# Kernel optimization log

Measured on AMD Instinct MI355X. Metric: run time of the kernel, lower is better.

The kernel has to match this reference:

```python
import jax, jax.numpy as jnp
import numpy as np

N = 500000      # gaussians
D = 256         # d_model
H = 8           # heads
DFF = 1024      # ffn hidden
L = 2           # encoder layers
VS = 0.0625     # voxel_size
MR = 10         # multires (both embedders)
EPS = 1e-5      # layernorm eps


def _embed(x, nf):
    freqs = 2.0 ** jnp.arange(nf, dtype=x.dtype)
    xf = x[..., None, :] * freqs[:, None]                  # [..., F, 3]
    sc = jnp.stack([jnp.sin(xf), jnp.cos(xf)], axis=-2)    # [..., F, 2, 3]
    return jnp.concatenate([x, sc.reshape(*x.shape[:-1], nf * 2 * 3)], axis=-1)


def _ln(x, w, b):
    m = x.mean(-1, keepdims=True)
    v = ((x - m) ** 2).mean(-1, keepdims=True)
    return (x - m) / jnp.sqrt(v + EPS) * w + b


def _mha(x, wi, bi, wo, bo):
    U, d = x.shape
    dh = d // H
    qkv = x @ wi.T + bi                                    # [U, 3d]
    q, k, v = jnp.split(qkv, 3, axis=-1)
    sp = lambda t: t.reshape(U, H, dh).transpose(1, 0, 2)  # [H, U, dh]
    q, k, v = sp(q), sp(k), sp(v)
    scale = 1.0 / jnp.sqrt(jnp.asarray(dh, x.dtype))
    attn = jax.nn.softmax(jnp.einsum('hqd,hkd->hqk', q, k) * scale, axis=-1)
    o = jnp.einsum('hqk,hkd->hqd', attn, v).transpose(1, 0, 2).reshape(U, d)
    return o @ wo.T + bo


def setup_inputs() -> dict:
    key = jax.random.key(0)
    ks = jax.random.split(key, 24)
    centres = jax.random.uniform(ks[0], (N, 3), dtype=jnp.float32)
    feats = jax.random.normal(ks[1], (N, D), dtype=jnp.float32)
    # voxelize + unique (data-dependent -> precompute, round() has zero grad anyway)
    vp = np.round(np.asarray(centres) / VS) * VS
    _, inv = np.unique(vp, axis=0, return_inverse=True)
    inv = inv.reshape(-1)
    U = int(inv.max()) + 1
    s = 0.02
    rn = lambda k, shp: jax.random.normal(k, shp, dtype=jnp.float32) * s
    PE = MR * 2 * 3 + 3  # 63
    return dict(
        gaussian_centres=centres,
        gaussian_features=feats,
        inverse_indices=jnp.asarray(inv, jnp.int32),
        num_unique=U,
        in_proj_w=rn(ks[2], (L, 3 * D, D)), in_proj_b=rn(ks[3], (L, 3 * D)),
        out_proj_w=rn(ks[4], (L, D, D)), out_proj_b=rn(ks[5], (L, D)),
        lin1_w=rn(ks[6], (L, DFF, D)), lin1_b=rn(ks[7], (L, DFF)),
        lin2_w=rn(ks[8], (L, D, DFF)), lin2_b=rn(ks[9], (L, D)),
        norm1_w=jnp.ones((L, D), jnp.float32), norm1_b=jnp.zeros((L, D), jnp.float32),
        norm2_w=jnp.ones((L, D), jnp.float32), norm2_b=jnp.zeros((L, D), jnp.float32),
        pe_w1=rn(ks[10], (D, PE)), pe_b1=rn(ks[11], (D,)),
        pe_w2=rn(ks[12], (D, D)), pe_b2=rn(ks[13], (D,)),
        dm_w1=rn(ks[14], (D, D + PE)), dm_b1=rn(ks[15], (D,)),
        dm_w2=rn(ks[16], (D, D)), dm_b2=rn(ks[17], (D,)),
    )


def reference(gaussian_centres, gaussian_features, inverse_indices, num_unique,
              in_proj_w, in_proj_b, out_proj_w, out_proj_b,
              lin1_w, lin1_b, lin2_w, lin2_b,
              norm1_w, norm1_b, norm2_w, norm2_b,
              pe_w1, pe_b1, pe_w2, pe_b2,
              dm_w1, dm_b1, dm_w2, dm_b2):
    # 1-4: voxelize + segment-sum features per unique voxel
    vp = jnp.round(gaussian_centres / VS) * VS
    agg = jax.ops.segment_sum(gaussian_features, inverse_indices, num_segments=num_unique)  # [U, D]
    uv = jnp.zeros((num_unique, 3), gaussian_centres.dtype).at[inverse_indices].set(vp)     # unique voxel coords
    # learnable positional encoding MLP
    pe = _embed(uv, MR)
    pe = jax.nn.leaky_relu(pe @ pe_w1.T + pe_b1, 0.01) @ pe_w2.T + pe_b2
    # transformer encoder (post-LN, relu, eval mode -> no dropout)
    x = agg + pe
    for l in range(L):
        x = _ln(x + _mha(x, in_proj_w[l], in_proj_b[l], out_proj_w[l], out_proj_b[l]),
                norm1_w[l], norm1_b[l])
        ff = jax.nn.relu(x @ lin1_w[l].T + lin1_b[l]) @ lin2_w[l].T + lin2_b[l]
        x = _ln(x + ff, norm2_w[l], norm2_b[l])
    # 6-7: gather back to per-gaussian rows
    rec = x[inverse_indices]                                # [N, D]
    # delta MLP: cat([pos_encoding, features])
    d_in = jnp.concatenate([_embed(gaussian_centres, MR), rec], axis=-1)
    delta = jax.nn.leaky_relu(d_in @ dm_w1.T + dm_b1, 0.01) @ dm_w2.T + dm_b2
    return rec + delta
```

## Files before the change

### kernel.cpp

```cpp
#include <hip/hip_runtime.h>
#include <math.h>

#define NG   500000
#define DM   256
#define NH   8
#define DHD  32
#define DFF  1024
#define NLAY 2
#define PED  63
#define VSF  0.0625f
#define EPSF 1e-5f
#define UP   4928
#define MAXU 4913
#define NQT  77
#define NDBLK 7813
#define SCL  0.17677669529663687f

typedef short bf16x8 __attribute__((ext_vector_type(8)));
typedef float f32x4 __attribute__((ext_vector_type(4)));

__device__ __forceinline__ float lrelu(float v){ return v >= 0.f ? v : 0.01f*v; }

__device__ __forceinline__ short f2b(float f){
  unsigned u = __float_as_uint(f);
  return (short)((u + 0x7fffu + ((u >> 16) & 1u)) >> 16);
}

__device__ __forceinline__ f32x4 mfma16(bf16x8 a, bf16x8 b, f32x4 c){
  return __builtin_amdgcn_mfma_f32_16x16x32_bf16(a, b, c, 0, 0, 0);
}

__device__ __forceinline__ float embed_elem(float cx, float cy, float cz, int j){
  if (j == 0) return cx;
  if (j == 1) return cy;
  if (j == 2) return cz;
  int q = j - 3;
  int f = q / 6;
  int r = q - f*6;
  int c = r % 3;
  float base = (c==0)?cx:((c==1)?cy:cz);
  float xf = base * (float)(1u << f);
  return (r < 3) ? sinf(xf) : cosf(xf);
}

__device__ __forceinline__ float wred(float v){
  #pragma unroll
  for (int o = 32; o > 0; o >>= 1) v += __shfl_xor(v, o);
  return v;
}

__global__ void zero_kernel(int* p, int n){
  int i = blockIdx.x*blockDim.x + threadIdx.x;
  if (i < n) p[i] = 0;
}

__global__ void prep_kernel(const float* __restrict__ centres, const int* __restrict__ inv,
                            int* __restrict__ counts, float* __restrict__ uv){
  for (int i = blockIdx.x*blockDim.x + threadIdx.x; i < NG; i += gridDim.x*blockDim.x){
    int v = inv[i];
    atomicAdd(&counts[v], 1);
    float vx = rintf(centres[i*3]   * 16.f) * VSF;
    float vy = rintf(centres[i*3+1] * 16.f) * VSF;
    float vz = rintf(centres[i*3+2] * 16.f) * VSF;
    uv[v*3] = vx; uv[v*3+1] = vy; uv[v*3+2] = vz;
  }
}

__global__ void scan_kernel(const int* __restrict__ counts, int* __restrict__ offs,
                            const int* __restrict__ pU){
  const int U = *pU;
  const int CH = 8;
  __shared__ int tot[1024];
  int tid = threadIdx.x;
  int base = tid * CH;
  int c[CH];
  int s = 0;
  #pragma unroll
  for (int i = 0; i < CH; ++i){
    int idx = base + i;
    int v = (idx < U) ? counts[idx] : 0;
    c[i] = s;
    s += v;
  }
  tot[tid] = s;
  __syncthreads();
  for (int o = 1; o < 1024; o <<= 1){
    int v = 0;
    if (tid >= o) v = tot[tid - o];
    __syncthreads();
    tot[tid] += v;
    __syncthreads();
  }
  int excl = tot[tid] - s;
  #pragma unroll
  for (int i = 0; i < CH; ++i){
    int idx = base + i;
    if (idx < U) offs[idx] = excl + c[i];
  }
}

__global__ void scatter_kernel(const int* __restrict__ inv, const int* __restrict__ offs,
                               int* __restrict__ cursor, int* __restrict__ gidx){
  for (int i = blockIdx.x*blockDim.x + threadIdx.x; i < NG; i += gridDim.x*blockDim.x){
    int v = inv[i];
    int p = atomicAdd(&cursor[v], 1);
    gidx[offs[v] + p] = i;
  }
}

__global__ void cvt_weights(const float* __restrict__ ipw, const float* __restrict__ opw,
                            const float* __restrict__ l1w, const float* __restrict__ l2w,
                            const float* __restrict__ dw1, const float* __restrict__ dw2,
                            short* ipwb, short* opwb, short* l1wb, short* l2wb,
                            short* dw2b, short* dw1bb, short* dw1ab){
  int i = blockIdx.x*256 + threadIdx.x;
  switch (blockIdx.y){
    case 0: if (i < 2*768*256)  ipwb[i] = f2b(ipw[i]); break;
    case 1: if (i < 2*256*256)  opwb[i] = f2b(opw[i]); break;
    case 2: if (i < 2*1024*256) l1wb[i] = f2b(l1w[i]); break;
    case 3: if (i < 2*256*1024) l2wb[i] = f2b(l2w[i]); break;
    case 4: if (i < 256*256)    dw2b[i] = f2b(dw2[i]); break;
    case 5: if (i < 256*256){ int r = i>>8, c = i&255; dw1bb[i] = f2b(dw1[r*319 + 63 + c]); } break;
    case 6: if (i < 256*64){  int r = i>>6, c = i&63;  dw1ab[i] = f2b(c < 63 ? dw1[r*319 + c] : 0.f); } break;
  }
}

__global__ __launch_bounds__(256) void agg_pe_kernel(const float* __restrict__ feats,
   const int* __restrict__ gidx, const int* __restrict__ offs, const int* __restrict__ counts,
   const float* __restrict__ uv, const float* __restrict__ pw1, const float* __restrict__ pb1,
   const float* __restrict__ pw2, const float* __restrict__ pb2,
   float* __restrict__ x, const int* __restrict__ pU){
  const int U = *pU;
  __shared__ int gl[512];
  __shared__ __align__(16) float4 red[256];
  __shared__ __align__(16) float e[PED];
  __shared__ __align__(16) float h[DM];
  const int t = threadIdx.x;
  const int c4 = t & 63;
  const int rr = t >> 6;
  for (int u = blockIdx.x; u < U; u += gridDim.x){
    const int o0 = offs[u], cnt = counts[u];
    float4 s = {0.f,0.f,0.f,0.f};
    for (int base = 0; base < cnt; base += 512){
      const int cc = min(cnt - base, 512);
      __syncthreads();
      for (int j = t; j < cc; j += 256) gl[j] = gidx[o0 + base + j];
      __syncthreads();
      int j = rr;
      for (; j + 8 <= cc; j += 8){
        const int r0 = gl[j], r1 = gl[j+4];
        float4 v0 = *reinterpret_cast<const float4*>(&feats[(size_t)r0*DM + c4*4]);
        float4 v1 = *reinterpret_cast<const float4*>(&feats[(size_t)r1*DM + c4*4]);
        s.x += v0.x + v1.x; s.y += v0.y + v1.y;
        s.z += v0.z + v1.z; s.w += v0.w + v1.w;
      }
      for (; j < cc; j += 4){
        float4 v0 = *reinterpret_cast<const float4*>(&feats[(size_t)gl[j]*DM + c4*4]);
        s.x += v0.x; s.y += v0.y; s.z += v0.z; s.w += v0.w;
      }
    }
    red[t] = s;
    if (t < PED)
      e[t] = embed_elem(uv[u*3], uv[u*3+1], uv[u*3+2], t);
    __syncthreads();
    if (rr == 0){
      float4 a = red[c4], b = red[64+c4], c = red[128+c4], d = red[192+c4];
      a.x += b.x + c.x + d.x; a.y += b.y + c.y + d.y;
      a.z += b.z + c.z + d.z; a.w += b.w + c.w + d.w;
      red[c4] = a;
    }
    __syncthreads();
    const float sum = reinterpret_cast<const float*>(red)[t];
    float a1 = pb1[t];
    const float* w1 = pw1 + t*PED;
    for (int k = 0; k < PED; ++k) a1 += w1[k]*e[k];
    h[t] = lrelu(a1);
    __syncthreads();
    float a2 = pb2[t];
    const float* w2 = pw2 + (size_t)t*DM;
    for (int k = 0; k < DM; k += 4){
      float4 w = *reinterpret_cast<const float4*>(w2+k);
      float4 hv = *reinterpret_cast<const float4*>(&h[k]);
      a2 += w.x*hv.x + w.y*hv.y + w.z*hv.z + w.w*hv.w;
    }
    x[(size_t)u*DM + t] = sum + a2;
    __syncthreads();
  }
}

template<int ACT, bool HASRES>
__global__ __launch_bounds__(256) void gemm_bf(const float* __restrict__ A,
    const short* __restrict__ Bbf, const float* __restrict__ bias,
    const float* __restrict__ res, float* __restrict__ C,
    const int K, const int Nn, const int* __restrict__ pU){
  const int M = *pU;
  const int r0 = blockIdx.x * 64;
  if (r0 >= M) return;
  const int n0 = blockIdx.y * 64;
  __shared__ __align__(16) short Al[64*32];
  const int tid = threadIdx.x;
  const int wid = tid >> 6, lane = tid & 63;
  const int l15 = lane & 15, l4 = lane >> 4;
  f32x4 acc[4];
  #pragma unroll
  for (int nt = 0; nt < 4; ++nt) acc[nt] = (f32x4){0.f,0.f,0.f,0.f};
  const int nk = K >> 5;
  const int srow = tid >> 2, se8 = (tid & 3) * 8;
  const int arowc = min(r0 + srow, M-1);
  for (int kc = 0; kc < nk; ++kc){
    {
      const float* ap = A + (size_t)arowc*K + kc*32 + se8;
      f32x4 a0 = *(const f32x4*)ap;
      f32x4 a1 = *(const f32x4*)(ap + 4);
      bf16x8 av;
      av[0]=f2b(a0[0]); av[1]=f2b(a0[1]); av[2]=f2b(a0[2]); av[3]=f2b(a0[3]);
      av[4]=f2b(a1[0]); av[5]=f2b(a1[1]); av[6]=f2b(a1[2]); av[7]=f2b(a1[3]);
      *(bf16x8*)&Al[(srow*32 + se8) ^ ((srow & 7) << 3)] = av;
    }
    __syncthreads();
    const int ar = 16*wid + l15;
    bf16x8 af = *(const bf16x8*)&Al[(ar*32 + 8*l4) ^ ((ar & 7) << 3)];
    #pragma unroll
    for (int nt = 0; nt < 4; ++nt){
      const short* bp = Bbf + (size_t)(n0 + 16*nt + l15)*K + kc*32 + 8*l4;
      bf16x8 bfr = *(const bf16x8*)bp;
      acc[nt] = mfma16(af, bfr, acc[nt]);
    }
    __syncthreads();
  }
  #pragma unroll
  for (int nt = 0; nt < 4; ++nt){
    const int col = n0 + 16*nt + l15;
    const float bv = bias[col];
    #pragma unroll
    for (int r = 0; r < 4; ++r){
      const int row = r0 + 16*wid + 4*l4 + r;
      if (row < M){
        float v = acc[nt][r] + bv;
        if (ACT == 1) v = fmaxf(v, 0.f);
        if (HASRES) v += res[(size_t)row*Nn + col];
        C[(size_t)row*Nn + col] = v;
      }
    }
  }
}

__global__ __launch_bounds__(256) void attn_mfma(const float* __restrict__ qkv,
                                                 float* __restrict__ y, const int* __restrict__ pU){
  const int U = *pU;
  const int bid = blockIdx.x;
  const int h = bid & 7, qt = bid >> 3;
  const int q0 = qt * 64;
  const int tid = threadIdx.x;
  const int wid = tid >> 6, lane = tid & 63;
  const int l15 = lane & 15, l4 = lane >> 4;
  __shared__ __align__(16) short Kl[64*32];
  __shared__ __align__(16) short Vt[32*64];
  __shared__ __align__(16) short Pl[4][64*16];

  const int qrow = min(q0 + 16*wid + l15, U-1);
  const float* qp = qkv + (size_t)qrow*768 + h*DHD + 8*l4;
  bf16x8 qf;
  {
    f32x4 q0v = *(const f32x4*)qp;
    f32x4 q1v = *(const f32x4*)(qp + 4);
    qf[0]=f2b(q0v[0]*SCL); qf[1]=f2b(q0v[1]*SCL); qf[2]=f2b(q0v[2]*SCL); qf[3]=f2b(q0v[3]*SCL);
    qf[4]=f2b(q1v[0]*SCL); qf[5]=f2b(q1v[1]*SCL); qf[6]=f2b(q1v[2]*SCL); qf[7]=f2b(q1v[3]*SCL);
  }
  f32x4 o0 = (f32x4){0.f,0.f,0.f,0.f}, o1 = (f32x4){0.f,0.f,0.f,0.f};
  float mrun = -INFINITY, lrun = 0.f;
  const int srow = tid >> 2, se8 = (tid & 3) * 8;
  const int ntile = (U + 63) >> 6;
  for (int kt = 0; kt < ntile; ++kt){
    const int kb = kt * 64;
    {
      const int krow = min(kb + srow, U-1);
      const float* kp = qkv + (size_t)krow*768 + DM + h*DHD + se8;
      f32x4 k0 = *(const f32x4*)kp;
      f32x4 k1 = *(const f32x4*)(kp + 4);
      bf16x8 kv;
      kv[0]=f2b(k0[0]); kv[1]=f2b(k0[1]); kv[2]=f2b(k0[2]); kv[3]=f2b(k0[3]);
      kv[4]=f2b(k1[0]); kv[5]=f2b(k1[1]); kv[6]=f2b(k1[2]); kv[7]=f2b(k1[3]);
      *(bf16x8*)&Kl[(srow*32 + se8) ^ ((srow & 7) << 3)] = kv;
      const float* vp = qkv + (size_t)krow*768 + 2*DM + h*DHD + se8;
      f32x4 v0 = *(const f32x4*)vp;
      f32x4 v1 = *(const f32x4*)(vp + 4);
      #pragma unroll
      for (int j = 0; j < 8; ++j){
        const int d = se8 + j;
        const float vv = (j < 4) ? v0[j & 3] : v1[j & 3];
        Vt[(d*64 + srow) ^ ((d & 7) << 3)] = f2b(vv);
      }
    }
    __syncthreads();
    float s[16];
    #pragma unroll
    for (int nt = 0; nt < 4; ++nt){
      const int row = 16*nt + l15;
      bf16x8 kf = *(const bf16x8*)&Kl[(row*32 + 8*l4) ^ ((row & 7) << 3)];
      f32x4 d = mfma16(kf, qf, (f32x4){0.f,0.f,0.f,0.f});
      const int kbase = kb + 16*nt + 4*l4;
      #pragma unroll
      for (int r = 0; r < 4; ++r)
        s[nt*4 + r] = (kbase + r < U) ? d[r] : -INFINITY;
    }
    float cm = s[0];
    #pragma unroll
    for (int i = 1; i < 16; ++i) cm = fmaxf(cm, s[i]);
    cm = fmaxf(cm, __shfl_xor(cm, 16));
    cm = fmaxf(cm, __shfl_xor(cm, 32));
    const float mnew = fmaxf(mrun, cm);
    const float f = __expf(mrun - mnew);
    float ls = 0.f;
    #pragma unroll
    for (int i = 0; i < 16; ++i){ s[i] = __expf(s[i] - mnew); ls += s[i]; }
    ls += __shfl_xor(ls, 16);
    ls += __shfl_xor(ls, 32);
    lrun = lrun * f + ls;
    o0 = o0 * f; o1 = o1 * f;
    mrun = mnew;
    #pragma unroll
    for (int nt = 0; nt < 4; ++nt)
      #pragma unroll
      for (int r = 0; r < 4; ++r){
        const int row = 16*nt + 4*l4 + r;
        Pl[wid][(row*16 + l15) ^ (((row >> 2) & 3) << 2)] = f2b(s[nt*4 + r]);
      }
    __syncthreads();
    #pragma unroll
    for (int kc = 0; kc < 2; ++kc){
      bf16x8 pf;
      #pragma unroll
      for (int j = 0; j < 8; ++j){
        const int row = 32*kc + 8*l4 + j;
        pf[j] = Pl[wid][(row*16 + l15) ^ (((row >> 2) & 3) << 2)];
      }
      {
        const int row = l15;
        bf16x8 vf = *(const bf16x8*)&Vt[(row*64 + 32*kc + 8*l4) ^ ((row & 7) << 3)];
        o0 = mfma16(vf, pf, o0);
      }
      {
        const int row = 16 + l15;
        bf16x8 vf = *(const bf16x8*)&Vt[(row*64 + 32*kc + 8*l4) ^ ((row & 7) << 3)];
        o1 = mfma16(vf, pf, o1);
      }
    }
    __syncthreads();
  }
  const float invl = 1.f / lrun;
  const int qg = q0 + 16*wid + l15;
  if (qg < U){
    float* yp = y + (size_t)qg*DM + h*DHD;
    #pragma unroll
    for (int r = 0; r < 4; ++r){
      yp[4*l4 + r]      = o0[r] * invl;
      yp[16 + 4*l4 + r] = o1[r] * invl;
    }
  }
}

__global__ __launch_bounds__(256) void ln_kernel(const float* __restrict__ in,
    const float* __restrict__ w, const float* __restrict__ b,
    float* __restrict__ out, const int* __restrict__ pU){
  const int U = *pU;
  const int t = threadIdx.x;
  const int wid = t >> 6;
  __shared__ float red[4];
  for (int u = blockIdx.x; u < U; u += gridDim.x){
    float v = in[(size_t)u*DM + t];
    float s = wred(v);
    if ((t & 63) == 0) red[wid] = s;
    __syncthreads();
    float mean = (red[0]+red[1]+red[2]+red[3]) * (1.f/DM);
    __syncthreads();
    float d = v - mean;
    float sq = wred(d*d);
    if ((t & 63) == 0) red[wid] = sq;
    __syncthreads();
    float var = (red[0]+red[1]+red[2]+red[3]) * (1.f/DM);
    out[(size_t)u*DM + t] = d * (1.0f/sqrtf(var + EPSF)) * w[t] + b[t];
    __syncthreads();
  }
}

__global__ __launch_bounds__(256) void delta_mfma(const float* __restrict__ centres,
   const int* __restrict__ inv, const float* __restrict__ x, const float* __restrict__ rc,
   const short* __restrict__ w1abf, const short* __restrict__ w2bf,
   const float* __restrict__ db2, float* __restrict__ out){
  __shared__ __align__(16) float cs[64][3];
  __shared__ int ivl[64];
  __shared__ __align__(16) short el[64*64];
  __shared__ __align__(16) short hl[64*256];
  const int tid = threadIdx.x;
  const int wid = tid >> 6, lane = tid & 63;
  const int l15 = lane & 15, l4 = lane >> 4;
  const int g0 = blockIdx.x * 64;
  if (tid < 64){
    const int gid = min(g0 + tid, NG-1);
    cs[tid][0] = centres[gid*3];
    cs[tid][1] = centres[gid*3+1];
    cs[tid][2] = centres[gid*3+2];
    ivl[tid] = inv[gid];
  }
  __syncthreads();
  for (int i = tid; i < 64*64; i += 256){
    const int g = i >> 6, j = i & 63;
    const float v = (j < PED) ? embed_elem(cs[g][0], cs[g][1], cs[g][2], j) : 0.f;
    el[(g*64 + j) ^ ((g & 7) << 3)] = f2b(v);
  }
  __syncthreads();
  bf16x8 ef[2];
  #pragma unroll
  for (int kc = 0; kc < 2; ++kc){
    const int row = 16*wid + l15;
    ef[kc] = *(const bf16x8*)&el[(row*64 + kc*32 + 8*l4) ^ ((row & 7) << 3)];
  }
  const int glb = 16*wid + 4*l4;
  #pragma unroll
  for (int nt = 0; nt < 16; ++nt){
    f32x4 a;
    #pragma unroll
    for (int r = 0; r < 4; ++r)
      a[r] = rc[(size_t)ivl[glb + r]*DM + 16*nt + l15];
    #pragma unroll
    for (int kc = 0; kc < 2; ++kc){
      const bf16x8 bfr = *(const bf16x8*)&w1abf[(16*nt + l15)*64 + kc*32 + 8*l4];
      a = mfma16(ef[kc], bfr, a);
    }
    #pragma unroll
    for (int r = 0; r < 4; ++r){
      const int row = glb + r;
      hl[(row*256 + 16*nt + l15) ^ ((row & 7) << 3)] = f2b(lrelu(a[r]));
    }
  }
  __syncthreads();
  bf16x8 hf[8];
  #pragma unroll
  for (int kc = 0; kc < 8; ++kc){
    const int row = 16*wid + l15;
    hf[kc] = *(const bf16x8*)&hl[(row*256 + kc*32 + 8*l4) ^ ((row & 7) << 3)];
  }
  f32x4 acc[16];
  #pragma unroll
  for (int nt = 0; nt < 16; ++nt){
    const float bv = db2[16*nt + l15];
    #pragma unroll
    for (int r = 0; r < 4; ++r)
      acc[nt][r] = x[(size_t)ivl[glb + r]*DM + 16*nt + l15] + bv;
  }
  #pragma unroll
  for (int kc = 0; kc < 8; ++kc){
    #pragma unroll
    for (int nt = 0; nt < 16; ++nt){
      const bf16x8 bfr = *(const bf16x8*)&w2bf[(size_t)(16*nt + l15)*256 + kc*32 + 8*l4];
      acc[nt] = mfma16(hf[kc], bfr, acc[nt]);
    }
  }
  #pragma unroll
  for (int nt = 0; nt < 16; ++nt){
    #pragma unroll
    for (int r = 0; r < 4; ++r){
      const int g = g0 + glb + r;
      if (g < NG)
        out[(size_t)g*DM + 16*nt + l15] = acc[nt][r];
    }
  }
}

extern "C" void kernel_launch(void* const* d_in, const int* in_sizes, int n_in,
                              void* d_out, int out_size, void* d_ws, size_t ws_size,
                              hipStream_t stream){
  (void)in_sizes; (void)n_in; (void)out_size; (void)ws_size;
  const float* centres = (const float*)d_in[0];
  const float* feats   = (const float*)d_in[1];
  const int*   inv     = (const int*)d_in[2];
  const int*   pU      = (const int*)d_in[3];
  const float* ipw = (const float*)d_in[4];
  const float* ipb = (const float*)d_in[5];
  const float* opw = (const float*)d_in[6];
  const float* opb = (const float*)d_in[7];
  const float* l1w = (const float*)d_in[8];
  const float* l1b = (const float*)d_in[9];
  const float* l2w = (const float*)d_in[10];
  const float* l2b = (const float*)d_in[11];
  const float* n1w = (const float*)d_in[12];
  const float* n1b = (const float*)d_in[13];
  const float* n2w = (const float*)d_in[14];
  const float* n2b = (const float*)d_in[15];
  const float* pw1 = (const float*)d_in[16];
  const float* pb1 = (const float*)d_in[17];
  const float* pw2 = (const float*)d_in[18];
  const float* pb2 = (const float*)d_in[19];
  const float* dw1 = (const float*)d_in[20];
  const float* db1 = (const float*)d_in[21];
  const float* dw2 = (const float*)d_in[22];
  const float* db2 = (const float*)d_in[23];
  float* out = (float*)d_out;

  char* ws = (char*)d_ws;
  size_t off = 0;
  auto take = [&](size_t bytes)->char*{
    char* p = ws + off; off += (bytes + 255) & ~(size_t)255; return p;
  };
  float* xb   = (float*)take((size_t)UP*DM*4);
  float* yb   = (float*)take((size_t)UP*DM*4);
  float* big  = (float*)take((size_t)UP*DFF*4);
  float* rcb  = (float*)take((size_t)UP*DM*4);
  float* uv   = (float*)take((size_t)UP*3*4);
  int* counts = (int*)take((size_t)2*UP*4);
  int* cursor = counts + UP;
  int* offs   = (int*)take((size_t)UP*4);
  int* gidx   = (int*)take((size_t)NG*4);
  short* ipwbf  = (short*)take((size_t)2*768*256*2);
  short* opwbf  = (short*)take((size_t)2*256*256*2);
  short* l1wbf  = (short*)take((size_t)2*1024*256*2);
  short* l2wbf  = (short*)take((size_t)2*256*1024*2);
  short* dw2bf  = (short*)take((size_t)256*256*2);
  short* dw1bbf = (short*)take((size_t)256*256*2);
  short* dw1abf = (short*)take((size_t)256*64*2);

  zero_kernel<<<(2*UP + 255)/256, 256, 0, stream>>>(counts, 2*UP);
  prep_kernel<<<1024, 256, 0, stream>>>(centres, inv, counts, uv);
  scan_kernel<<<1, 1024, 0, stream>>>(counts, offs, pU);
  scatter_kernel<<<1024, 256, 0, stream>>>(inv, offs, cursor, gidx);
  cvt_weights<<<dim3(2048, 7), 256, 0, stream>>>(ipw, opw, l1w, l2w, dw1, dw2,
                                                 ipwbf, opwbf, l1wbf, l2wbf,
                                                 dw2bf, dw1bbf, dw1abf);
  agg_pe_kernel<<<MAXU, 256, 0, stream>>>(feats, gidx, offs, counts, uv,
                                          pw1, pb1, pw2, pb2, xb, pU);

  for (int l = 0; l < NLAY; ++l){
    gemm_bf<0,false><<<dim3(NQT,12), 256, 0, stream>>>(xb, ipwbf + (size_t)l*768*256,
        ipb + (size_t)l*768, nullptr, big, DM, 3*DM, pU);
    attn_mfma<<<8*NQT, 256, 0, stream>>>(big, yb, pU);
    gemm_bf<0,true><<<dim3(NQT,4), 256, 0, stream>>>(yb, opwbf + (size_t)l*256*256,
        opb + (size_t)l*DM, xb, big, DM, DM, pU);
    ln_kernel<<<1024, 256, 0, stream>>>(big, n1w + (size_t)l*DM, n1b + (size_t)l*DM, xb, pU);
    gemm_bf<1,false><<<dim3(NQT,16), 256, 0, stream>>>(xb, l1wbf + (size_t)l*1024*256,
        l1b + (size_t)l*DFF, nullptr, big, DM, DFF, pU);
    gemm_bf<0,true><<<dim3(NQT,4), 256, 0, stream>>>(big, l2wbf + (size_t)l*256*1024,
        l2b + (size_t)l*DM, xb, yb, DFF, DM, pU);
    ln_kernel<<<1024, 256, 0, stream>>>(yb, n2w + (size_t)l*DM, n2b + (size_t)l*DM, xb, pU);
  }

  gemm_bf<0,false><<<dim3(NQT,4), 256, 0, stream>>>(xb, dw1bbf, db1, nullptr, rcb, DM, DM, pU);
  delta_mfma<<<NDBLK, 256, 0, stream>>>(centres, inv, xb, rcb, dw1abf, dw2bf, db2, out);
}
```

Measured before the change: 2.654 ms.

## Process gaussians in voxel-sorted order in delta kernel and compute embedding in registers

The delta kernel now walks gaussians through the gidx permutation, which groups them by voxel, so the per-row gathers of rc and x hit a few voxel rows per block and get better cache reuse. Outputs are scattered back to the original gaussian indices. The positional embedding is computed directly into MFMA operand registers instead of going through an LDS staging buffer and an extra barrier. The second GEMM is split into two halves of 8 accumulators to cut register pressure. In exchange, the output stores become scattered rows instead of contiguous block writes, and each lane now computes the sin/cos embedding itself.

```diff
diff --git a/kernel.cpp b/kernel.cpp
--- a/kernel.cpp
+++ b/kernel.cpp
@@ -385,44 +385,48 @@
 }
 
 __global__ __launch_bounds__(256) void delta_mfma(const float* __restrict__ centres,
-   const int* __restrict__ inv, const float* __restrict__ x, const float* __restrict__ rc,
+   const int* __restrict__ inv, const int* __restrict__ gidx,
+   const float* __restrict__ x, const float* __restrict__ rc,
    const short* __restrict__ w1abf, const short* __restrict__ w2bf,
    const float* __restrict__ db2, float* __restrict__ out){
   __shared__ __align__(16) float cs[64][3];
   __shared__ int ivl[64];
-  __shared__ __align__(16) short el[64*64];
+  __shared__ int sg[64];
   __shared__ __align__(16) short hl[64*256];
   const int tid = threadIdx.x;
   const int wid = tid >> 6, lane = tid & 63;
   const int l15 = lane & 15, l4 = lane >> 4;
-  const int g0 = blockIdx.x * 64;
+  const int p0 = blockIdx.x * 64;
   if (tid < 64){
-    const int gid = min(g0 + tid, NG-1);
+    const int pos = p0 + tid;
+    const int gid = gidx[min(pos, NG-1)];
+    sg[tid]  = (pos < NG) ? gid : -1;
+    ivl[tid] = inv[gid];
     cs[tid][0] = centres[gid*3];
     cs[tid][1] = centres[gid*3+1];
     cs[tid][2] = centres[gid*3+2];
-    ivl[tid] = inv[gid];
   }
   __syncthreads();
-  for (int i = tid; i < 64*64; i += 256){
-    const int g = i >> 6, j = i & 63;
-    const float v = (j < PED) ? embed_elem(cs[g][0], cs[g][1], cs[g][2], j) : 0.f;
-    el[(g*64 + j) ^ ((g & 7) << 3)] = f2b(v);
-  }
-  __syncthreads();
+  const int arow = 16*wid + l15;
+  const float cx = cs[arow][0], cy = cs[arow][1], cz = cs[arow][2];
   bf16x8 ef[2];
   #pragma unroll
-  for (int kc = 0; kc < 2; ++kc){
-    const int row = 16*wid + l15;
-    ef[kc] = *(const bf16x8*)&el[(row*64 + kc*32 + 8*l4) ^ ((row & 7) << 3)];
-  }
+  for (int kc = 0; kc < 2; ++kc)
+    #pragma unroll
+    for (int jj = 0; jj < 8; ++jj){
+      const int j = kc*32 + 8*l4 + jj;
+      ef[kc][jj] = f2b(j < PED ? embed_elem(cx, cy, cz, j) : 0.f);
+    }
   const int glb = 16*wid + 4*l4;
+  const int rv0 = ivl[glb], rv1 = ivl[glb+1], rv2 = ivl[glb+2], rv3 = ivl[glb+3];
   #pragma unroll
   for (int nt = 0; nt < 16; ++nt){
+    const int c = 16*nt + l15;
     f32x4 a;
-    #pragma unroll
-    for (int r = 0; r < 4; ++r)
-      a[r] = rc[(size_t)ivl[glb + r]*DM + 16*nt + l15];
+    a[0] = rc[(size_t)rv0*DM + c];
+    a[1] = rc[(size_t)rv1*DM + c];
+    a[2] = rc[(size_t)rv2*DM + c];
+    a[3] = rc[(size_t)rv3*DM + c];
     #pragma unroll
     for (int kc = 0; kc < 2; ++kc){
       const bf16x8 bfr = *(const bf16x8*)&w1abf[(16*nt + l15)*64 + kc*32 + 8*l4];
@@ -431,7 +435,7 @@
     #pragma unroll
     for (int r = 0; r < 4; ++r){
       const int row = glb + r;
-      hl[(row*256 + 16*nt + l15) ^ ((row & 7) << 3)] = f2b(lrelu(a[r]));
+      hl[(row*256 + c) ^ ((row & 7) << 3)] = f2b(lrelu(a[r]));
     }
   }
   __syncthreads();
@@ -441,29 +445,34 @@
     const int row = 16*wid + l15;
     hf[kc] = *(const bf16x8*)&hl[(row*256 + kc*32 + 8*l4) ^ ((row & 7) << 3)];
   }
-  f32x4 acc[16];
-  #pragma unroll
-  for (int nt = 0; nt < 16; ++nt){
-    const float bv = db2[16*nt + l15];
-    #pragma unroll
-    for (int r = 0; r < 4; ++r)
-      acc[nt][r] = x[(size_t)ivl[glb + r]*DM + 16*nt + l15] + bv;
-  }
-  #pragma unroll
-  for (int kc = 0; kc < 8; ++kc){
-    #pragma unroll
-    for (int nt = 0; nt < 16; ++nt){
-      const bf16x8 bfr = *(const bf16x8*)&w2bf[(size_t)(16*nt + l15)*256 + kc*32 + 8*l4];
-      acc[nt] = mfma16(hf[kc], bfr, acc[nt]);
-    }
-  }
-  #pragma unroll
-  for (int nt = 0; nt < 16; ++nt){
-    #pragma unroll
-    for (int r = 0; r < 4; ++r){
-      const int g = g0 + glb + r;
-      if (g < NG)
-        out[(size_t)g*DM + 16*nt + l15] = acc[nt][r];
+  const int g0 = sg[glb], g1 = sg[glb+1], g2 = sg[glb+2], g3 = sg[glb+3];
+  #pragma unroll
+  for (int half = 0; half < 2; ++half){
+    f32x4 acc[8];
+    #pragma unroll
+    for (int q = 0; q < 8; ++q){
+      const int c = half*128 + 16*q + l15;
+      const float bv = db2[c];
+      acc[q][0] = x[(size_t)rv0*DM + c] + bv;
+      acc[q][1] = x[(size_t)rv1*DM + c] + bv;
+      acc[q][2] = x[(size_t)rv2*DM + c] + bv;
+      acc[q][3] = x[(size_t)rv3*DM + c] + bv;
+    }
+    #pragma unroll
+    for (int kc = 0; kc < 8; ++kc)
+      #pragma unroll
+      for (int q = 0; q < 8; ++q){
+        const int n = half*128 + 16*q + l15;
+        const bf16x8 bfr = *(const bf16x8*)&w2bf[(size_t)n*256 + kc*32 + 8*l4];
+        acc[q] = mfma16(hf[kc], bfr, acc[q]);
+      }
+    #pragma unroll
+    for (int q = 0; q < 8; ++q){
+      const int c = half*128 + 16*q + l15;
+      if (g0 >= 0) out[(size_t)g0*DM + c] = acc[q][0];
+      if (g1 >= 0) out[(size_t)g1*DM + c] = acc[q][1];
+      if (g2 >= 0) out[(size_t)g2*DM + c] = acc[q][2];
+      if (g3 >= 0) out[(size_t)g3*DM + c] = acc[q][3];
     }
   }
 }
@@ -545,5 +554,5 @@
   }
 
   gemm_bf<0,false><<<dim3(NQT,4), 256, 0, stream>>>(xb, dw1bbf, db1, nullptr, rcb, DM, DM, pU);
-  delta_mfma<<<NDBLK, 256, 0, stream>>>(centres, inv, xb, rcb, dw1abf, dw2bf, db2, out);
-}
+  delta_mfma<<<NDBLK, 256, 0, stream>>>(centres, inv, gidx, xb, rcb, dw1abf, dw2bf, db2, out);
+}
```

Result: faster. 2.473 ms (-6.8%).
